# Kernel optimization log

Measured on AMD Instinct MI355X. Metric: run time of the kernel, lower is better.

Reference implementation:

```python
import jax, jax.numpy as jnp
import numpy as np

B, Hh, Ww, C = 64, 14, 14, 2048   # batch, feat map H, W, encoder_dim
E, D, A, V, L = 512, 512, 512, 30000, 32  # embed, decoder, attn dims, vocab, max text len
SC = 0.02


def setup_inputs() -> dict:
    key = jax.random.key(0)
    ks = jax.random.split(key, 16)
    def p(k, shape):
        return jax.random.normal(k, shape, jnp.float32) * SC
    lens = jax.random.randint(ks[2], (B, 1), 2, L + 1).at[0, 0].set(L)  # ensure max len present -> static T
    return {
        "encoder_out": jax.random.normal(ks[0], (B, Hh, Ww, C), jnp.float32),
        "encoded_text": jax.random.randint(ks[1], (B, L), 0, V),
        "encoded_text_len": lens,
        "W_init_h": p(ks[3], (C, D)), "b_init_h": jnp.zeros((D,), jnp.float32),
        "W_init_c": p(ks[4], (C, D)), "b_init_c": jnp.zeros((D,), jnp.float32),
        "W_en": p(ks[5], (C, A)), "b_en": jnp.zeros((A,), jnp.float32),
        "W_de": p(ks[6], (D, A)), "b_de": jnp.zeros((A,), jnp.float32),
        "W_at": p(ks[7], (A, 1)), "b_at": jnp.zeros((1,), jnp.float32),
        "W_gate": p(ks[8], (D, C)), "b_gate": jnp.zeros((C,), jnp.float32),
        "W_ih": p(ks[9], (C + E, 4 * D)), "b_ih": jnp.zeros((4 * D,), jnp.float32),
        "W_hh": p(ks[10], (D, 4 * D)), "b_hh": jnp.zeros((4 * D,), jnp.float32),
        "embed_table": p(ks[11], (V, E)),
        "W_head": p(ks[12], (D, V)), "b_head": jnp.zeros((V,), jnp.float32),
    }


def reference(encoder_out, encoded_text, encoded_text_len,
              W_init_h, b_init_h, W_init_c, b_init_c,
              W_en, b_en, W_de, b_de, W_at, b_at,
              W_gate, b_gate, W_ih, b_ih, W_hh, b_hh,
              embed_table, W_head, b_head):
    b, hh, ww, c = encoder_out.shape
    img = encoder_out.reshape(b, hh * ww, c)          # [b, p, c]
    img_mean = img.mean(axis=1)
    # NOTE: original computes h0/c0 on UNSORTED img and never reindexes them (repo quirk); reproduced faithfully.
    h0 = img_mean @ W_init_h + b_init_h               # [b, d]
    c0 = img_mean @ W_init_c + b_init_c
    tl = encoded_text_len[:, 0]
    idx = jnp.argsort(-tl, stable=True)               # descending stable sort
    img_s = img[idx]
    text_s = encoded_text[idx]
    tlen = tl[idx] - 1                                # decode steps per example
    T = encoded_text.shape[1] - 1                     # static: one row has full length L
    emb = embed_table[text_s[:, :T]]                  # [b, T, e]
    en_attn = img_s @ W_en + b_en                     # [b, p, a] time-invariant attn projection

    def step(carry, xs):
        h, cst = carry
        emb_t, mask = xs                              # [b,e], [b]
        de = h @ W_de + b_de                          # [b, a]
        score = (jax.nn.relu(en_attn + de[:, None, :]) @ W_at)[..., 0] + b_at[0]  # [b, p]
        alpha = jax.nn.softmax(score, axis=1)
        ctx = jnp.einsum('bp,bpc->bc', alpha, img_s)
        gate = jax.nn.sigmoid(h @ W_gate + b_gate)
        x = jnp.concatenate([ctx * gate, emb_t], axis=1)
        gates = x @ W_ih + b_ih + h @ W_hh + b_hh     # [b, 4d], torch LSTMCell gate order i,f,g,o
        i, f, g, o = jnp.split(gates, 4, axis=1)
        c_new = jax.nn.sigmoid(f) * cst + jax.nn.sigmoid(i) * jnp.tanh(g)
        h_new = jax.nn.sigmoid(o) * jnp.tanh(c_new)
        m = mask[:, None]
        h = jnp.where(m, h_new, h)
        cst = jnp.where(m, c_new, cst)
        pred = jnp.where(m, h_new @ W_head + b_head, 0.0)  # dropout in eval mode = identity
        attn = jnp.where(m, alpha, 0.0)
        return (h, cst), (pred, attn)

    emb_T = jnp.swapaxes(emb, 0, 1)                   # [T, b, e]
    masks = jnp.arange(T)[:, None] < tlen[None, :]    # [T, b] prefix-active (lengths sorted desc)
    (_, _), (preds, attns) = jax.lax.scan(step, (h0, c0), (emb_T, masks))
    prediction = jnp.swapaxes(preds, 0, 1)            # [b, T, V]
    attention = jnp.swapaxes(attns, 0, 1)             # [b, T, p]
    return prediction, text_s, tlen, attention, idx
```

## Files before the change

kernel.cpp:

```cpp
#include <hip/hip_runtime.h>
#include <hip/hip_bf16.h>
#include <math.h>

#define BB 64
#define PP 196
#define CC 2048
#define DD 512
#define AA 512
#define EE 512
#define VV 30000
#define VPAD 30016
#define LL 32
#define TT 31
#define XH 2560
#define HEADBLK 469

typedef short bf16x8 __attribute__((ext_vector_type(8)));
typedef float f32x4 __attribute__((ext_vector_type(4)));

__device__ inline unsigned short f2bf(float x) {
    __hip_bfloat16 h = __float2bfloat16(x);
    return __builtin_bit_cast(unsigned short, h);
}
__device__ inline float bf2f(unsigned short u) {
    unsigned int x = ((unsigned int)u) << 16;
    return __builtin_bit_cast(float, x);
}

template<int K, int LDA>
__device__ inline void mm4(const unsigned short* __restrict__ a0,
                           const unsigned short* __restrict__ b0,
                           f32x4 acc[4]) {
#pragma unroll
    for (int kc = 0; kc < K / 32; ++kc) {
        bf16x8 bfr = *reinterpret_cast<const bf16x8*>(b0 + kc * 32);
#pragma unroll
        for (int mt = 0; mt < 4; ++mt) {
            bf16x8 afr = *reinterpret_cast<const bf16x8*>(a0 + (size_t)mt * 16 * LDA + kc * 32);
            acc[mt] = __builtin_amdgcn_mfma_f32_16x16x32_bf16(afr, bfr, acc[mt], 0, 0, 0);
        }
    }
}


__global__ void k_sort(const int* __restrict__ text, const int* __restrict__ lens,
                       int* __restrict__ idx, int* __restrict__ inv, int* __restrict__ tlen,
                       int* __restrict__ ts,
                       float* __restrict__ out_text, float* __restrict__ out_tlen,
                       float* __restrict__ out_idx) {
    int j = threadIdx.x;
    __shared__ int key[BB];
    __shared__ int sidx[BB];
    key[j] = lens[j];
    __syncthreads();
    int kj = key[j];
    int pos = 0;
    for (int q = 0; q < BB; ++q) {
        int kq = key[q];
        if (kq > kj || (kq == kj && q < j)) pos++;
    }
    sidx[pos] = j;
    __syncthreads();
    int src = sidx[j];
    idx[j] = src;
    inv[src] = j;
    int tl = key[src] - 1;
    tlen[j] = tl;
    out_idx[j] = (float)src;
    out_tlen[j] = (float)tl;
    for (int l = 0; l < LL; ++l) {
        int tok = text[src * LL + l];
        ts[j * LL + l] = tok;
        out_text[j * LL + l] = (float)tok;
    }
}

__global__ __launch_bounds__(256) void k_cvtenc(const float* __restrict__ enc, const int* __restrict__ idx,
                                                unsigned short* __restrict__ enc_bf) {
    int row = blockIdx.x;
    int bs = row / PP, p = row - bs * PP;
    int c0 = threadIdx.x * 8;
    const float* src = enc + ((size_t)idx[bs] * PP + p) * CC + c0;
    f32x4 lo = *reinterpret_cast<const f32x4*>(src);
    f32x4 hi = *reinterpret_cast<const f32x4*>(src + 4);
    unsigned short* dst = enc_bf + (size_t)row * CC + c0;
    bf16x8 v;
    v[0] = (short)f2bf(lo[0]); v[1] = (short)f2bf(lo[1]);
    v[2] = (short)f2bf(lo[2]); v[3] = (short)f2bf(lo[3]);
    v[4] = (short)f2bf(hi[0]); v[5] = (short)f2bf(hi[1]);
    v[6] = (short)f2bf(hi[2]); v[7] = (short)f2bf(hi[3]);
    *reinterpret_cast<bf16x8*>(dst) = v;
}

__global__ __launch_bounds__(256) void k_meanbf(const unsigned short* __restrict__ enc_bf,
                                                const int* __restrict__ inv,
                                                unsigned short* __restrict__ mean_bf) {
    int b = blockIdx.x;
    int lane = threadIdx.x & 31, pg = threadIdx.x >> 5;
    int c0 = blockIdx.y * 256 + lane * 8;
    const unsigned short* img = enc_bf + (size_t)inv[b] * PP * CC + c0;
    float s[8] = {0.f, 0.f, 0.f, 0.f, 0.f, 0.f, 0.f, 0.f};
    for (int p = pg; p < PP; p += 8) {
        bf16x8 v = *reinterpret_cast<const bf16x8*>(img + (size_t)p * CC);
#pragma unroll
        for (int j = 0; j < 8; ++j) s[j] += bf2f((unsigned short)v[j]);
    }
    __shared__ float red[8][256];
#pragma unroll
    for (int j = 0; j < 8; ++j) red[pg][lane * 8 + j] = s[j];
    __syncthreads();
    int c = threadIdx.x;
    float tt = 0.f;
#pragma unroll
    for (int g = 0; g < 8; ++g) tt += red[g][c];
    mean_bf[(size_t)b * CC + blockIdx.y * 256 + c] = f2bf(tt * (1.0f / PP));
}

__global__ __launch_bounds__(64) void k_init_mfma(const unsigned short* __restrict__ mean_bf,
                                                  const unsigned short* __restrict__ Wt_ih,
                                                  const unsigned short* __restrict__ Wt_ic,
                                                  const float* __restrict__ bh, const float* __restrict__ bc,
                                                  unsigned short* __restrict__ xh_bf, float* __restrict__ c_f32) {
    int isC = blockIdx.x >= 32;
    int n0 = (blockIdx.x & 31) * 16;
    int lane = threadIdx.x;
    const unsigned short* Wt = isC ? Wt_ic : Wt_ih;
    const unsigned short* a0 = mean_bf + (size_t)(lane & 15) * CC + ((lane >> 4) * 8);
    const unsigned short* b0 = Wt + (size_t)(n0 + (lane & 15)) * CC + ((lane >> 4) * 8);
    f32x4 acc[4];
#pragma unroll
    for (int mt = 0; mt < 4; ++mt) acc[mt] = (f32x4){0.f, 0.f, 0.f, 0.f};
    mm4<CC, CC>(a0, b0, acc);
    int n = n0 + (lane & 15);
    float bv = (isC ? bc : bh)[n];
#pragma unroll
    for (int mt = 0; mt < 4; ++mt)
#pragma unroll
        for (int r = 0; r < 4; ++r) {
            int m = mt * 16 + (lane >> 4) * 4 + r;
            float val = acc[mt][r] + bv;
            if (isC) c_f32[(size_t)m * DD + n] = val;
            else     xh_bf[(size_t)m * XH + CC + n] = f2bf(val);
        }
}

__global__ __launch_bounds__(256) void k_transcvt(const float* __restrict__ src, int K, int N,
                                                  unsigned short* __restrict__ dst, int dstStride, int Npad) {
    __shared__ float t[32][33];
    int n0 = blockIdx.x * 32, k0 = blockIdx.y * 32;
    int tx = threadIdx.x, ty = threadIdx.y;
#pragma unroll
    for (int r = 0; r < 4; ++r) {
        int k = k0 + ty + r * 8;
        int n = n0 + tx;
        t[ty + r * 8][tx] = (n < N) ? src[(size_t)k * N + n] : 0.f;
    }
    __syncthreads();
#pragma unroll
    for (int r = 0; r < 4; ++r) {
        int n = n0 + ty + r * 8;
        int k = k0 + tx;
        if (n < Npad) dst[(size_t)n * dstStride + k] = f2bf(t[tx][ty + r * 8]);
    }
}

__global__ __launch_bounds__(256) void k_emball(const float* __restrict__ embed, const int* __restrict__ ts,
                                                unsigned short* __restrict__ emb_all) {
    int row = blockIdx.x;
    int t = row >> 6, b = row & 63;
    int tok = ts[b * LL + t];
    int e = threadIdx.x * 2;
    const float* src = embed + (size_t)tok * EE + e;
    unsigned short* dst = emb_all + (size_t)row * EE + e;
    dst[0] = f2bf(src[0]);
    dst[1] = f2bf(src[1]);
}

__global__ __launch_bounds__(256) void k_embw(const unsigned short* __restrict__ emb_all,
                                              const unsigned short* __restrict__ Wt_emb,
                                              const float* __restrict__ bih, const float* __restrict__ bhh,
                                              float* __restrict__ embW) {
    int tstep = blockIdx.x;
    int n0 = blockIdx.y * 64;
    int lane = threadIdx.x & 63, w = threadIdx.x >> 6;
    const unsigned short* a0 = emb_all + ((size_t)tstep * 64 + (lane & 15)) * EE + ((lane >> 4) * 8);
    const unsigned short* b0 = Wt_emb + (size_t)(n0 + w * 16 + (lane & 15)) * EE + ((lane >> 4) * 8);
    f32x4 acc[4];
#pragma unroll
    for (int mt = 0; mt < 4; ++mt) acc[mt] = (f32x4){0.f, 0.f, 0.f, 0.f};
    mm4<EE, EE>(a0, b0, acc);
    int n = n0 + w * 16 + (lane & 15);
    float bv = bih[n] + bhh[n];
#pragma unroll
    for (int mt = 0; mt < 4; ++mt)
#pragma unroll
        for (int r = 0; r < 4; ++r) {
            int m = mt * 16 + (lane >> 4) * 4 + r;
            embW[((size_t)tstep * 64 + m) * 2048 + n] = acc[mt][r] + bv;
        }
}

__global__ __launch_bounds__(256) void k_enattn_mfma(const unsigned short* __restrict__ enc_bf,
                                                     const unsigned short* __restrict__ Wt,
                                                     const float* __restrict__ bias,
                                                     unsigned short* __restrict__ en_bf) {
    int m0 = blockIdx.x * 64;
    int lane = threadIdx.x & 63, w = threadIdx.x >> 6;
    const unsigned short* a0 = enc_bf + (size_t)(m0 + (lane & 15)) * CC + ((lane >> 4) * 8);
    const unsigned short* bptr[8];
#pragma unroll
    for (int nt = 0; nt < 8; ++nt) {
        int rowB = nt * 64 + w * 16 + (lane & 15);
        bptr[nt] = Wt + (size_t)rowB * CC + ((lane >> 4) * 8);
    }
    f32x4 acc[4][8];
#pragma unroll
    for (int mt = 0; mt < 4; ++mt)
#pragma unroll
        for (int nt = 0; nt < 8; ++nt) acc[mt][nt] = (f32x4){0.f, 0.f, 0.f, 0.f};

    for (int kc = 0; kc < CC / 32; ++kc) {
        bf16x8 afr[4];
#pragma unroll
        for (int mt = 0; mt < 4; ++mt)
            afr[mt] = *reinterpret_cast<const bf16x8*>(a0 + (size_t)mt * 16 * CC + kc * 32);
#pragma unroll
        for (int nt = 0; nt < 8; ++nt) {
            bf16x8 bfr = *reinterpret_cast<const bf16x8*>(bptr[nt] + kc * 32);
#pragma unroll
            for (int mt = 0; mt < 4; ++mt)
                acc[mt][nt] = __builtin_amdgcn_mfma_f32_16x16x32_bf16(afr[mt], bfr, acc[mt][nt], 0, 0, 0);
        }
    }
#pragma unroll
    for (int nt = 0; nt < 8; ++nt) {
        int n = nt * 64 + w * 16 + (lane & 15);
        float bv = bias[n];
#pragma unroll
        for (int mt = 0; mt < 4; ++mt)
#pragma unroll
            for (int r = 0; r < 4; ++r) {
                int m = m0 + mt * 16 + (lane >> 4) * 4 + r;
                en_bf[(size_t)m * AA + n] = f2bf(acc[mt][nt][r] + bv);
            }
    }
}


__global__ __launch_bounds__(256) void k_de0(const unsigned short* __restrict__ xh_bf,
                                             const unsigned short* __restrict__ Wt,
                                             const float* __restrict__ bias, float* __restrict__ de) {
    int lane = threadIdx.x & 63, w = threadIdx.x >> 6;
    int n0 = (blockIdx.x * 4 + w) * 16;
    const unsigned short* a0 = xh_bf + CC + (size_t)(lane & 15) * XH + ((lane >> 4) * 8);
    const unsigned short* b0 = Wt + (size_t)(n0 + (lane & 15)) * DD + ((lane >> 4) * 8);
    f32x4 acc[4];
#pragma unroll
    for (int mt = 0; mt < 4; ++mt) acc[mt] = (f32x4){0.f, 0.f, 0.f, 0.f};
    mm4<DD, XH>(a0, b0, acc);
    int n = n0 + (lane & 15);
    float bv = bias[n];
#pragma unroll
    for (int mt = 0; mt < 4; ++mt)
#pragma unroll
        for (int r = 0; r < 4; ++r) {
            int m = mt * 16 + (lane >> 4) * 4 + r;
            de[(size_t)m * AA + n] = acc[mt][r] + bv;
        }
}

__global__ __launch_bounds__(256) void k_score(const unsigned short* __restrict__ en_bf,
                                               const float* __restrict__ de,
                                               const float* __restrict__ Wat, const float* __restrict__ bat,
                                               const int* __restrict__ tlen, int t,
                                               float* __restrict__ alpha, float* __restrict__ out_attn) {
    int b = blockIdx.x;
    int tid = threadIdx.x;
    __shared__ float deL[AA];
    __shared__ float watL[AA];
    __shared__ float red[256];
    deL[tid] = de[(size_t)b * AA + tid];
    deL[tid + 256] = de[(size_t)b * AA + 256 + tid];
    watL[tid] = Wat[tid];
    watL[tid + 256] = Wat[tid + 256];
    __syncthreads();
    float s0 = 0.f, s1 = 0.f;
    if (tid < PP) {
        const unsigned short* er = en_bf + ((size_t)b * PP + tid) * AA;
#pragma unroll 2
        for (int a16 = 0; a16 < AA / 16; ++a16) {
            bf16x8 v0 = *reinterpret_cast<const bf16x8*>(er + a16 * 16);
            bf16x8 v1 = *reinterpret_cast<const bf16x8*>(er + a16 * 16 + 8);
#pragma unroll
            for (int j = 0; j < 8; ++j) {
                float u0 = fmaxf(bf2f((unsigned short)v0[j]) + deL[a16 * 16 + j], 0.f);
                float u1 = fmaxf(bf2f((unsigned short)v1[j]) + deL[a16 * 16 + 8 + j], 0.f);
                s0 = fmaf(u0, watL[a16 * 16 + j], s0);
                s1 = fmaf(u1, watL[a16 * 16 + 8 + j], s1);
            }
        }
    }
    float s = s0 + s1 + bat[0];
    red[tid] = (tid < PP) ? s : -3.4e38f;
    __syncthreads();
    for (int st = 128; st > 0; st >>= 1) {
        if (tid < st) red[tid] = fmaxf(red[tid], red[tid + st]);
        __syncthreads();
    }
    float m = red[0];
    __syncthreads();
    float e = (tid < PP) ? expf(s - m) : 0.f;
    red[tid] = e;
    __syncthreads();
    for (int st = 128; st > 0; st >>= 1) {
        if (tid < st) red[tid] += red[tid + st];
        __syncthreads();
    }
    float inv = 1.0f / red[0];
    if (tid < PP) {
        float al = e * inv;
        alpha[(size_t)b * PP + tid] = al;
        bool act = t < tlen[b];
        out_attn[((size_t)b * TT + t) * PP + tid] = act ? al : 0.f;
    }
}

__global__ __launch_bounds__(256) void k_ctx(const unsigned short* __restrict__ enc_bf,
                                             const float* __restrict__ alpha, float* __restrict__ ctx) {
    int b = blockIdx.x;
    int lane = threadIdx.x & 31, pg = threadIdx.x >> 5;
    int c0 = blockIdx.y * 256 + lane * 8;
    __shared__ float al[PP];
    if (threadIdx.x < PP) al[threadIdx.x] = alpha[(size_t)b * PP + threadIdx.x];
    __syncthreads();
    const unsigned short* img = enc_bf + (size_t)b * PP * CC + c0;
    float s[8] = {0.f, 0.f, 0.f, 0.f, 0.f, 0.f, 0.f, 0.f};
    for (int p = pg; p < PP; p += 8) {
        float a = al[p];
        bf16x8 v = *reinterpret_cast<const bf16x8*>(img + (size_t)p * CC);
#pragma unroll
        for (int j = 0; j < 8; ++j) s[j] = fmaf(a, bf2f((unsigned short)v[j]), s[j]);
    }
    __shared__ float red[8][256];
#pragma unroll
    for (int j = 0; j < 8; ++j) red[pg][lane * 8 + j] = s[j];
    __syncthreads();
    int c = threadIdx.x;
    float tt = 0.f;
#pragma unroll
    for (int g = 0; g < 8; ++g) tt += red[g][c];
    ctx[(size_t)b * CC + blockIdx.y * 256 + c] = tt;
}

__global__ __launch_bounds__(64) void k_gatex_mfma(unsigned short* __restrict__ xh_bf,
                                                   const unsigned short* __restrict__ Wt,
                                                   const float* __restrict__ bias,
                                                   const float* __restrict__ ctx) {
    int n0 = blockIdx.x * 16;
    int lane = threadIdx.x;
    const unsigned short* a0 = xh_bf + CC + (size_t)(lane & 15) * XH + ((lane >> 4) * 8);
    const unsigned short* b0 = Wt + (size_t)(n0 + (lane & 15)) * DD + ((lane >> 4) * 8);
    f32x4 acc[4];
#pragma unroll
    for (int mt = 0; mt < 4; ++mt) acc[mt] = (f32x4){0.f, 0.f, 0.f, 0.f};
    mm4<DD, XH>(a0, b0, acc);
    int n = n0 + (lane & 15);
    float bv = bias[n];
#pragma unroll
    for (int mt = 0; mt < 4; ++mt)
#pragma unroll
        for (int r = 0; r < 4; ++r) {
            int m = mt * 16 + (lane >> 4) * 4 + r;
            float g = 1.f / (1.f + expf(-(acc[mt][r] + bv)));
            xh_bf[(size_t)m * XH + n] = f2bf(ctx[(size_t)m * CC + n] * g);
        }
}

__global__ __launch_bounds__(64) void k_gateslstm(const unsigned short* __restrict__ xh_bf,
                                                  const unsigned short* __restrict__ Wt,
                                                  const float* __restrict__ embW,
                                                  const int* __restrict__ tlen, int t,
                                                  unsigned short* __restrict__ xh_out,
                                                  float* __restrict__ c_f32,
                                                  unsigned short* __restrict__ hn_bf) {
    int d0 = blockIdx.x * 16;
    int lane = threadIdx.x;
    int col = lane & 15;
    const unsigned short* a0 = xh_bf + (size_t)col * XH + ((lane >> 4) * 8);
    const unsigned short* bptr[4];
#pragma unroll
    for (int g = 0; g < 4; ++g)
        bptr[g] = Wt + (size_t)(g * DD + d0 + col) * XH + ((lane >> 4) * 8);

    f32x4 acc[4][4];
    const float* ew = embW + (size_t)t * 64 * 2048;
#pragma unroll
    for (int g = 0; g < 4; ++g)
#pragma unroll
        for (int mt = 0; mt < 4; ++mt)
#pragma unroll
            for (int r = 0; r < 4; ++r) {
                int m = mt * 16 + (lane >> 4) * 4 + r;
                acc[g][mt][r] = ew[(size_t)m * 2048 + g * DD + d0 + col];
            }

#pragma unroll 4
    for (int kc = 0; kc < XH / 32; ++kc) {
        bf16x8 afr[4];
#pragma unroll
        for (int mt = 0; mt < 4; ++mt)
            afr[mt] = *reinterpret_cast<const bf16x8*>(a0 + (size_t)mt * 16 * XH + kc * 32);
#pragma unroll
        for (int g = 0; g < 4; ++g) {
            bf16x8 bfr = *reinterpret_cast<const bf16x8*>(bptr[g] + kc * 32);
#pragma unroll
            for (int mt = 0; mt < 4; ++mt)
                acc[g][mt] = __builtin_amdgcn_mfma_f32_16x16x32_bf16(afr[mt], bfr, acc[g][mt], 0, 0, 0);
        }
    }

    int d = d0 + col;
#pragma unroll
    for (int mt = 0; mt < 4; ++mt)
#pragma unroll
        for (int r = 0; r < 4; ++r) {
            int b = mt * 16 + (lane >> 4) * 4 + r;
            float iv = acc[0][mt][r], fv = acc[1][mt][r], gv = acc[2][mt][r], ov = acc[3][mt][r];
            float cv = c_f32[(size_t)b * DD + d];
            float si = 1.f / (1.f + expf(-iv));
            float sf = 1.f / (1.f + expf(-fv));
            float so = 1.f / (1.f + expf(-ov));
            float cn = sf * cv + si * tanhf(gv);
            float hn = so * tanhf(cn);
            hn_bf[(size_t)b * DD + d] = f2bf(hn);
            if (t < tlen[b]) {
                xh_out[(size_t)b * XH + CC + d] = f2bf(hn);
                c_f32[(size_t)b * DD + d] = cn;
            }
        }
}

__global__ __launch_bounds__(256) void k_head_de(const unsigned short* __restrict__ hn_bf,
                                                 const unsigned short* __restrict__ Wt_head,
                                                 const float* __restrict__ b_head,
                                                 const unsigned short* __restrict__ xh_bf,
                                                 const unsigned short* __restrict__ Wt_de,
                                                 const float* __restrict__ b_de,
                                                 const int* __restrict__ tlen, int t,
                                                 float* __restrict__ out_pred, float* __restrict__ de) {
    int lane = threadIdx.x & 63, w = threadIdx.x >> 6;
    if (blockIdx.x < HEADBLK) {
        int n0 = blockIdx.x * 64;
        const unsigned short* a0 = hn_bf + (size_t)(lane & 15) * DD + ((lane >> 4) * 8);
        const unsigned short* b0 = Wt_head + (size_t)(n0 + w * 16 + (lane & 15)) * DD + ((lane >> 4) * 8);
        f32x4 acc[4];
#pragma unroll
        for (int mt = 0; mt < 4; ++mt) acc[mt] = (f32x4){0.f, 0.f, 0.f, 0.f};
        mm4<DD, DD>(a0, b0, acc);
        int v = n0 + w * 16 + (lane & 15);
        if (v >= VV) return;
        float bv = b_head[v];
#pragma unroll
        for (int mt = 0; mt < 4; ++mt)
#pragma unroll
            for (int r = 0; r < 4; ++r) {
                int b = mt * 16 + (lane >> 4) * 4 + r;
                bool act = t < tlen[b];
                out_pred[(size_t)b * TT * VV + (size_t)t * VV + v] = act ? (acc[mt][r] + bv) : 0.f;
            }
    } else {
        int n0 = ((blockIdx.x - HEADBLK) * 4 + w) * 16;
        const unsigned short* a0 = xh_bf + CC + (size_t)(lane & 15) * XH + ((lane >> 4) * 8);
        const unsigned short* b0 = Wt_de + (size_t)(n0 + (lane & 15)) * DD + ((lane >> 4) * 8);
        f32x4 acc[4];
#pragma unroll
        for (int mt = 0; mt < 4; ++mt) acc[mt] = (f32x4){0.f, 0.f, 0.f, 0.f};
        mm4<DD, XH>(a0, b0, acc);
        int n = n0 + (lane & 15);
        float bv = b_de[n];
#pragma unroll
        for (int mt = 0; mt < 4; ++mt)
#pragma unroll
            for (int r = 0; r < 4; ++r) {
                int m = mt * 16 + (lane >> 4) * 4 + r;
                de[(size_t)m * AA + n] = acc[mt][r] + bv;
            }
    }
}

extern "C" void kernel_launch(void* const* d_in, const int* in_sizes, int n_in,
                              void* d_out, int out_size, void* d_ws, size_t ws_size,
                              hipStream_t stream) {
    const float* enc     = (const float*)d_in[0];
    const int*   text    = (const int*)d_in[1];
    const int*   lens    = (const int*)d_in[2];
    const float* W_init_h = (const float*)d_in[3];
    const float* b_init_h = (const float*)d_in[4];
    const float* W_init_c = (const float*)d_in[5];
    const float* b_init_c = (const float*)d_in[6];
    const float* W_en    = (const float*)d_in[7];
    const float* b_en    = (const float*)d_in[8];
    const float* W_de    = (const float*)d_in[9];
    const float* b_de    = (const float*)d_in[10];
    const float* W_at    = (const float*)d_in[11];
    const float* b_at    = (const float*)d_in[12];
    const float* W_gate  = (const float*)d_in[13];
    const float* b_gate  = (const float*)d_in[14];
    const float* W_ih    = (const float*)d_in[15];
    const float* b_ih    = (const float*)d_in[16];
    const float* W_hh    = (const float*)d_in[17];
    const float* b_hh    = (const float*)d_in[18];
    const float* embed   = (const float*)d_in[19];
    const float* W_head  = (const float*)d_in[20];
    const float* b_head  = (const float*)d_in[21];

    float* outf = (float*)d_out;
    float* out_pred = outf;
    float* out_text = outf + (size_t)BB * TT * VV;
    float* out_tlen = out_text + BB * LL;
    float* out_attn = out_tlen + BB;
    float* out_idx  = out_attn + (size_t)BB * TT * PP;

    char* wsb = (char*)d_ws;
    int* idx  = (int*)wsb;
    int* inv  = idx + 64;
    int* tlen = inv + 64;
    int* ts   = tlen + 64;
    float* fw = (float*)(wsb + 16384);
    float* c_f32 = fw;  fw += (size_t)BB * DD;
    float* de    = fw;  fw += (size_t)BB * AA;
    float* alpha = fw;  fw += (size_t)BB * PP;
    float* ctx   = fw;  fw += (size_t)BB * CC;
    float* embW  = fw;  fw += (size_t)TT * BB * 2048;
    unsigned short* us = (unsigned short*)fw;
    unsigned short* mean_bf = us;  us += (size_t)BB * CC;
    unsigned short* xh_bf   = us;  us += (size_t)BB * XH;
    unsigned short* hn_bf   = us;  us += (size_t)BB * DD;
    unsigned short* emb_all = us;  us += (size_t)TT * BB * EE;
    unsigned short* en_bf   = us;  us += (size_t)BB * PP * AA;
    unsigned short* enc_bf  = us;  us += (size_t)BB * PP * CC;
    unsigned short* Wt_en   = us;  us += (size_t)AA * CC;
    unsigned short* Wt_de   = us;  us += (size_t)AA * DD;
    unsigned short* Wt_gate = us;  us += (size_t)CC * DD;
    unsigned short* Wt_emb  = us;  us += (size_t)2048 * EE;
    unsigned short* Wt_ihh  = us;  us += (size_t)2048 * XH;
    unsigned short* Wt_ih0  = us;  us += (size_t)DD * CC;
    unsigned short* Wt_ic0  = us;  us += (size_t)DD * CC;
    unsigned short* Wt_head = us;  us += (size_t)VPAD * DD;

    k_sort<<<1, 64, 0, stream>>>(text, lens, idx, inv, tlen, ts, out_text, out_tlen, out_idx);
    k_cvtenc<<<BB * PP, 256, 0, stream>>>(enc, idx, enc_bf);
    k_meanbf<<<dim3(BB, CC / 256), 256, 0, stream>>>(enc_bf, inv, mean_bf);

    dim3 tb(32, 8);
    k_transcvt<<<dim3(AA / 32, CC / 32), tb, 0, stream>>>(W_en, CC, AA, Wt_en, CC, AA);
    k_transcvt<<<dim3(AA / 32, DD / 32), tb, 0, stream>>>(W_de, DD, AA, Wt_de, DD, AA);
    k_transcvt<<<dim3(CC / 32, DD / 32), tb, 0, stream>>>(W_gate, DD, CC, Wt_gate, DD, CC);
    k_transcvt<<<dim3(CC / 32, CC / 32), tb, 0, stream>>>(W_ih, CC, 2048, Wt_ihh, XH, 2048);
    k_transcvt<<<dim3(CC / 32, DD / 32), tb, 0, stream>>>(W_hh, DD, 2048, Wt_ihh + CC, XH, 2048);
    k_transcvt<<<dim3(CC / 32, DD / 32), tb, 0, stream>>>(W_ih + (size_t)CC * 2048, DD, 2048, Wt_emb, EE, 2048);
    k_transcvt<<<dim3(DD / 32, CC / 32), tb, 0, stream>>>(W_init_h, CC, DD, Wt_ih0, CC, DD);
    k_transcvt<<<dim3(DD / 32, CC / 32), tb, 0, stream>>>(W_init_c, CC, DD, Wt_ic0, CC, DD);
    k_transcvt<<<dim3(VPAD / 32, DD / 32), tb, 0, stream>>>(W_head, DD, VV, Wt_head, DD, VPAD);

    k_init_mfma<<<64, 64, 0, stream>>>(mean_bf, Wt_ih0, Wt_ic0, b_init_h, b_init_c, xh_bf, c_f32);
    k_emball<<<TT * BB, 256, 0, stream>>>(embed, ts, emb_all);
    k_embw<<<dim3(TT, 2048 / 64), 256, 0, stream>>>(emb_all, Wt_emb, b_ih, b_hh, embW);
    k_enattn_mfma<<<PP, 256, 0, stream>>>(enc_bf, Wt_en, b_en, en_bf);
    k_de0<<<8, 256, 0, stream>>>(xh_bf, Wt_de, b_de, de);

    for (int t = 0; t < TT; ++t) {
        k_score<<<BB, 256, 0, stream>>>(en_bf, de, W_at, b_at, tlen, t, alpha, out_attn);
        k_ctx<<<dim3(BB, 8), 256, 0, stream>>>(enc_bf, alpha, ctx);
        k_gatex_mfma<<<CC / 16, 64, 0, stream>>>(xh_bf, Wt_gate, b_gate, ctx);
        k_gateslstm<<<DD / 16, 64, 0, stream>>>(xh_bf, Wt_ihh, embW, tlen, t, xh_bf, c_f32, hn_bf);
        k_head_de<<<HEADBLK + 8, 256, 0, stream>>>(hn_bf, Wt_head, b_head, xh_bf, Wt_de, b_de,
                                                   tlen, t, out_pred, de);
    }
}
```

Measured before the change: 3.091 ms.

## Fuse attention score, softmax and context; skip inactive rows in per-step GEMMs

```diff
diff --git a/kernel.cpp b/kernel.cpp
--- a/kernel.cpp
+++ b/kernel.cpp
@@ -38,6 +38,23 @@
         for (int mt = 0; mt < 4; ++mt) {
             bf16x8 afr = *reinterpret_cast<const bf16x8*>(a0 + (size_t)mt * 16 * LDA + kc * 32);
             acc[mt] = __builtin_amdgcn_mfma_f32_16x16x32_bf16(afr, bfr, acc[mt], 0, 0, 0);
+        }
+    }
+}
+
+template<int K, int LDA>
+__device__ inline void mm4s(const unsigned short* __restrict__ a0,
+                            const unsigned short* __restrict__ b0,
+                            const bool act[4], f32x4 acc[4]) {
+#pragma unroll 4
+    for (int kc = 0; kc < K / 32; ++kc) {
+        bf16x8 bfr = *reinterpret_cast<const bf16x8*>(b0 + kc * 32);
+#pragma unroll
+        for (int mt = 0; mt < 4; ++mt) {
+            if (act[mt]) {
+                bf16x8 afr = *reinterpret_cast<const bf16x8*>(a0 + (size_t)mt * 16 * LDA + kc * 32);
+                acc[mt] = __builtin_amdgcn_mfma_f32_16x16x32_bf16(afr, bfr, acc[mt], 0, 0, 0);
+            }
         }
     }
 }
@@ -246,71 +263,103 @@
     }
 }
 
-
-__global__ __launch_bounds__(256) void k_de0(const unsigned short* __restrict__ xh_bf,
-                                             const unsigned short* __restrict__ Wt,
-                                             const float* __restrict__ bias, float* __restrict__ de) {
+__global__ __launch_bounds__(256) void k_pre0(const unsigned short* __restrict__ xh_bf,
+                                              const unsigned short* __restrict__ Wt_de,
+                                              const float* __restrict__ b_de,
+                                              const unsigned short* __restrict__ Wt_gate,
+                                              const float* __restrict__ b_gate,
+                                              float* __restrict__ de, float* __restrict__ gsig) {
     int lane = threadIdx.x & 63, w = threadIdx.x >> 6;
-    int n0 = (blockIdx.x * 4 + w) * 16;
-    const unsigned short* a0 = xh_bf + CC + (size_t)(lane & 15) * XH + ((lane >> 4) * 8);
-    const unsigned short* b0 = Wt + (size_t)(n0 + (lane & 15)) * DD + ((lane >> 4) * 8);
+    int l15 = lane & 15, hi = lane >> 4;
+    const unsigned short* a0 = xh_bf + CC + (size_t)l15 * XH + hi * 8;
     f32x4 acc[4];
 #pragma unroll
     for (int mt = 0; mt < 4; ++mt) acc[mt] = (f32x4){0.f, 0.f, 0.f, 0.f};
-    mm4<DD, XH>(a0, b0, acc);
-    int n = n0 + (lane & 15);
-    float bv = bias[n];
-#pragma unroll
-    for (int mt = 0; mt < 4; ++mt)
-#pragma unroll
-        for (int r = 0; r < 4; ++r) {
-            int m = mt * 16 + (lane >> 4) * 4 + r;
-            de[(size_t)m * AA + n] = acc[mt][r] + bv;
-        }
-}
-
-__global__ __launch_bounds__(256) void k_score(const unsigned short* __restrict__ en_bf,
+    if (blockIdx.x < 8) {
+        int n0 = (blockIdx.x * 4 + w) * 16;
+        const unsigned short* b0 = Wt_de + (size_t)(n0 + l15) * DD + hi * 8;
+        mm4<DD, XH>(a0, b0, acc);
+        int n = n0 + l15;
+        float bv = b_de[n];
+#pragma unroll
+        for (int mt = 0; mt < 4; ++mt)
+#pragma unroll
+            for (int r = 0; r < 4; ++r) {
+                int m = mt * 16 + hi * 4 + r;
+                de[(size_t)m * AA + n] = acc[mt][r] + bv;
+            }
+    } else {
+        int n0 = (blockIdx.x - 8) * 64 + w * 16;
+        const unsigned short* b0 = Wt_gate + (size_t)(n0 + l15) * DD + hi * 8;
+        mm4<DD, XH>(a0, b0, acc);
+        int n = n0 + l15;
+        float bv = b_gate[n];
+#pragma unroll
+        for (int mt = 0; mt < 4; ++mt)
+#pragma unroll
+            for (int r = 0; r < 4; ++r) {
+                int m = mt * 16 + hi * 4 + r;
+                gsig[(size_t)m * CC + n] = 1.f / (1.f + expf(-(acc[mt][r] + bv)));
+            }
+    }
+}
+
+
+__global__ __launch_bounds__(1024) void k_attn(const unsigned short* __restrict__ en_bf,
                                                const float* __restrict__ de,
                                                const float* __restrict__ Wat, const float* __restrict__ bat,
                                                const int* __restrict__ tlen, int t,
-                                               float* __restrict__ alpha, float* __restrict__ out_attn) {
-    int b = blockIdx.x;
-    int tid = threadIdx.x;
+                                               const unsigned short* __restrict__ enc_bf,
+                                               const float* __restrict__ gsig,
+                                               unsigned short* __restrict__ xh_bf,
+                                               float* __restrict__ out_attn) {
+    int b = blockIdx.x, tid = threadIdx.x;
+    if (t >= tlen[b]) {
+        if (tid < PP) out_attn[((size_t)b * TT + t) * PP + tid] = 0.f;
+        return;
+    }
     __shared__ float deL[AA];
     __shared__ float watL[AA];
+    __shared__ float sred[256][4];
+    __shared__ float sL[256];
     __shared__ float red[256];
-    deL[tid] = de[(size_t)b * AA + tid];
-    deL[tid + 256] = de[(size_t)b * AA + 256 + tid];
-    watL[tid] = Wat[tid];
-    watL[tid + 256] = Wat[tid + 256];
-    __syncthreads();
-    float s0 = 0.f, s1 = 0.f;
-    if (tid < PP) {
-        const unsigned short* er = en_bf + ((size_t)b * PP + tid) * AA;
-#pragma unroll 2
-        for (int a16 = 0; a16 < AA / 16; ++a16) {
-            bf16x8 v0 = *reinterpret_cast<const bf16x8*>(er + a16 * 16);
-            bf16x8 v1 = *reinterpret_cast<const bf16x8*>(er + a16 * 16 + 8);
+    __shared__ float red4[4][2048];
+    if (tid < 512) { deL[tid] = de[(size_t)b * AA + tid]; watL[tid] = Wat[tid]; }
+    __syncthreads();
+    int row = tid >> 2, ch = tid & 3;
+    float s = 0.f;
+    if (row < PP) {
+        const unsigned short* er = en_bf + ((size_t)b * PP + row) * AA + ch * 128;
+#pragma unroll
+        for (int a8 = 0; a8 < 16; ++a8) {
+            bf16x8 v = *reinterpret_cast<const bf16x8*>(er + a8 * 8);
 #pragma unroll
             for (int j = 0; j < 8; ++j) {
-                float u0 = fmaxf(bf2f((unsigned short)v0[j]) + deL[a16 * 16 + j], 0.f);
-                float u1 = fmaxf(bf2f((unsigned short)v1[j]) + deL[a16 * 16 + 8 + j], 0.f);
-                s0 = fmaf(u0, watL[a16 * 16 + j], s0);
-                s1 = fmaf(u1, watL[a16 * 16 + 8 + j], s1);
-            }
-        }
-    }
-    float s = s0 + s1 + bat[0];
-    red[tid] = (tid < PP) ? s : -3.4e38f;
+                int ix = ch * 128 + a8 * 8 + j;
+                float u = fmaxf(bf2f((unsigned short)v[j]) + deL[ix], 0.f);
+                s = fmaf(u, watL[ix], s);
+            }
+        }
+    }
+    sred[row][ch] = s;
+    __syncthreads();
+    float sc = 0.f;
+    if (tid < 256) {
+        sc = sred[tid][0] + sred[tid][1] + sred[tid][2] + sred[tid][3] + bat[0];
+        red[tid] = (tid < PP) ? sc : -3.4e38f;
+    }
     __syncthreads();
     for (int st = 128; st > 0; st >>= 1) {
         if (tid < st) red[tid] = fmaxf(red[tid], red[tid + st]);
         __syncthreads();
     }
-    float m = red[0];
-    __syncthreads();
-    float e = (tid < PP) ? expf(s - m) : 0.f;
-    red[tid] = e;
+    float mx = red[0];
+    __syncthreads();
+    if (tid < 256) {
+        float e = (tid < PP) ? expf(sc - mx) : 0.f;
+        sL[tid] = e;
+        red[tid] = e;
+    }
     __syncthreads();
     for (int st = 128; st > 0; st >>= 1) {
         if (tid < st) red[tid] += red[tid + st];
@@ -318,172 +367,160 @@
     }
     float inv = 1.0f / red[0];
     if (tid < PP) {
-        float al = e * inv;
-        alpha[(size_t)b * PP + tid] = al;
-        bool act = t < tlen[b];
-        out_attn[((size_t)b * TT + t) * PP + tid] = act ? al : 0.f;
-    }
-}
-
-__global__ __launch_bounds__(256) void k_ctx(const unsigned short* __restrict__ enc_bf,
-                                             const float* __restrict__ alpha, float* __restrict__ ctx) {
-    int b = blockIdx.x;
-    int lane = threadIdx.x & 31, pg = threadIdx.x >> 5;
-    int c0 = blockIdx.y * 256 + lane * 8;
-    __shared__ float al[PP];
-    if (threadIdx.x < PP) al[threadIdx.x] = alpha[(size_t)b * PP + threadIdx.x];
-    __syncthreads();
+        float al = sL[tid] * inv;
+        sL[tid] = al;
+        out_attn[((size_t)b * TT + t) * PP + tid] = al;
+    }
+    __syncthreads();
+    int lane8 = tid & 255, pg = tid >> 8;
+    int c0 = lane8 * 8;
     const unsigned short* img = enc_bf + (size_t)b * PP * CC + c0;
-    float s[8] = {0.f, 0.f, 0.f, 0.f, 0.f, 0.f, 0.f, 0.f};
-    for (int p = pg; p < PP; p += 8) {
-        float a = al[p];
+    float s8[8] = {0.f, 0.f, 0.f, 0.f, 0.f, 0.f, 0.f, 0.f};
+    for (int p = pg; p < PP; p += 4) {
+        float a = sL[p];
         bf16x8 v = *reinterpret_cast<const bf16x8*>(img + (size_t)p * CC);
 #pragma unroll
-        for (int j = 0; j < 8; ++j) s[j] = fmaf(a, bf2f((unsigned short)v[j]), s[j]);
-    }
-    __shared__ float red[8][256];
-#pragma unroll
-    for (int j = 0; j < 8; ++j) red[pg][lane * 8 + j] = s[j];
-    __syncthreads();
-    int c = threadIdx.x;
-    float tt = 0.f;
-#pragma unroll
-    for (int g = 0; g < 8; ++g) tt += red[g][c];
-    ctx[(size_t)b * CC + blockIdx.y * 256 + c] = tt;
-}
-
-__global__ __launch_bounds__(64) void k_gatex_mfma(unsigned short* __restrict__ xh_bf,
+        for (int j = 0; j < 8; ++j) s8[j] = fmaf(a, bf2f((unsigned short)v[j]), s8[j]);
+    }
+#pragma unroll
+    for (int j = 0; j < 8; ++j) red4[pg][c0 + j] = s8[j];
+    __syncthreads();
+    for (int c = tid; c < CC; c += 1024) {
+        float v = red4[0][c] + red4[1][c] + red4[2][c] + red4[3][c];
+        xh_bf[(size_t)b * XH + c] = f2bf(v * gsig[(size_t)b * CC + c]);
+    }
+}
+
+__global__ __launch_bounds__(256) void k_gateslstm(const unsigned short* __restrict__ xh_bf,
                                                    const unsigned short* __restrict__ Wt,
-                                                   const float* __restrict__ bias,
-                                                   const float* __restrict__ ctx) {
-    int n0 = blockIdx.x * 16;
-    int lane = threadIdx.x;
-    const unsigned short* a0 = xh_bf + CC + (size_t)(lane & 15) * XH + ((lane >> 4) * 8);
-    const unsigned short* b0 = Wt + (size_t)(n0 + (lane & 15)) * DD + ((lane >> 4) * 8);
+                                                   const float* __restrict__ embW,
+                                                   const int* __restrict__ tlen, int t,
+                                                   unsigned short* __restrict__ xh_out,
+                                                   float* __restrict__ c_f32,
+                                                   unsigned short* __restrict__ hn_bf) {
+    int d0 = blockIdx.x * 16;
+    int tid = threadIdx.x, wid = tid >> 6, lane = tid & 63;
+    int l15 = lane & 15, hi = lane >> 4;
+    bool act[4];
+#pragma unroll
+    for (int mt = 0; mt < 4; ++mt) act[mt] = t < tlen[mt * 16];
+
+    const unsigned short* a0 = xh_bf + (size_t)l15 * XH + hi * 8;
+    const unsigned short* b0 = Wt + (size_t)(wid * DD + d0 + l15) * XH + hi * 8;
+
     f32x4 acc[4];
+    const float* ew = embW + (size_t)t * 64 * 2048;
+#pragma unroll
+    for (int mt = 0; mt < 4; ++mt)
+#pragma unroll
+        for (int r = 0; r < 4; ++r) {
+            int m = mt * 16 + hi * 4 + r;
+            acc[mt][r] = ew[(size_t)m * 2048 + wid * DD + d0 + l15];
+        }
+    mm4s<XH, XH>(a0, b0, act, acc);
+
+    __shared__ float lg[4][64][16];
+#pragma unroll
+    for (int mt = 0; mt < 4; ++mt)
+#pragma unroll
+        for (int r = 0; r < 4; ++r) lg[wid][lane][mt * 4 + r] = acc[mt][r];
+    __syncthreads();
+    if (wid == 0) {
+        int d = d0 + l15;
+#pragma unroll
+        for (int mt = 0; mt < 4; ++mt) {
+            if (!act[mt]) continue;
+#pragma unroll
+            for (int r = 0; r < 4; ++r) {
+                int b = mt * 16 + hi * 4 + r;
+                float iv = lg[0][lane][mt * 4 + r];
+                float fv = lg[1][lane][mt * 4 + r];
+                float gv = lg[2][lane][mt * 4 + r];
+                float ov = lg[3][lane][mt * 4 + r];
+                float cv = c_f32[(size_t)b * DD + d];
+                float si = 1.f / (1.f + expf(-iv));
+                float sf = 1.f / (1.f + expf(-fv));
+                float so = 1.f / (1.f + expf(-ov));
+                float cn = sf * cv + si * tanhf(gv);
+                float hn = so * tanhf(cn);
+                hn_bf[(size_t)b * DD + d] = f2bf(hn);
+                if (t < tlen[b]) {
+                    xh_out[(size_t)b * XH + CC + d] = f2bf(hn);
+                    c_f32[(size_t)b * DD + d] = cn;
+                }
+            }
+        }
+    }
+}
+
+__global__ __launch_bounds__(256) void k_head_de_gate(const unsigned short* __restrict__ hn_bf,
+                                                      const unsigned short* __restrict__ Wt_head,
+                                                      const float* __restrict__ b_head,
+                                                      const unsigned short* __restrict__ xh_bf,
+                                                      const unsigned short* __restrict__ Wt_de,
+                                                      const float* __restrict__ b_de,
+                                                      const unsigned short* __restrict__ Wt_gate,
+                                                      const float* __restrict__ b_gate,
+                                                      const int* __restrict__ tlen, int t,
+                                                      float* __restrict__ out_pred,
+                                                      float* __restrict__ de, float* __restrict__ gsig) {
+    int lane = threadIdx.x & 63, w = threadIdx.x >> 6;
+    int l15 = lane & 15, hi = lane >> 4;
+    f32x4 acc[4];
 #pragma unroll
     for (int mt = 0; mt < 4; ++mt) acc[mt] = (f32x4){0.f, 0.f, 0.f, 0.f};
-    mm4<DD, XH>(a0, b0, acc);
-    int n = n0 + (lane & 15);
-    float bv = bias[n];
-#pragma unroll
-    for (int mt = 0; mt < 4; ++mt)
-#pragma unroll
-        for (int r = 0; r < 4; ++r) {
-            int m = mt * 16 + (lane >> 4) * 4 + r;
-            float g = 1.f / (1.f + expf(-(acc[mt][r] + bv)));
-            xh_bf[(size_t)m * XH + n] = f2bf(ctx[(size_t)m * CC + n] * g);
-        }
-}
-
-__global__ __launch_bounds__(64) void k_gateslstm(const unsigned short* __restrict__ xh_bf,
-                                                  const unsigned short* __restrict__ Wt,
-                                                  const float* __restrict__ embW,
-                                                  const int* __restrict__ tlen, int t,
-                                                  unsigned short* __restrict__ xh_out,
-                                                  float* __restrict__ c_f32,
-                                                  unsigned short* __restrict__ hn_bf) {
-    int d0 = blockIdx.x * 16;
-    int lane = threadIdx.x;
-    int col = lane & 15;
-    const unsigned short* a0 = xh_bf + (size_t)col * XH + ((lane >> 4) * 8);
-    const unsigned short* bptr[4];
-#pragma unroll
-    for (int g = 0; g < 4; ++g)
-        bptr[g] = Wt + (size_t)(g * DD + d0 + col) * XH + ((lane >> 4) * 8);
-
-    f32x4 acc[4][4];
-    const float* ew = embW + (size_t)t * 64 * 2048;
-#pragma unroll
-    for (int g = 0; g < 4; ++g)
-#pragma unroll
-        for (int mt = 0; mt < 4; ++mt)
-#pragma unroll
-            for (int r = 0; r < 4; ++r) {
-                int m = mt * 16 + (lane >> 4) * 4 + r;
-                acc[g][mt][r] = ew[(size_t)m * 2048 + g * DD + d0 + col];
-            }
-
-#pragma unroll 4
-    for (int kc = 0; kc < XH / 32; ++kc) {
-        bf16x8 afr[4];
-#pragma unroll
-        for (int mt = 0; mt < 4; ++mt)
-            afr[mt] = *reinterpret_cast<const bf16x8*>(a0 + (size_t)mt * 16 * XH + kc * 32);
-#pragma unroll
-        for (int g = 0; g < 4; ++g) {
-            bf16x8 bfr = *reinterpret_cast<const bf16x8*>(bptr[g] + kc * 32);
-#pragma unroll
-            for (int mt = 0; mt < 4; ++mt)
-                acc[g][mt] = __builtin_amdgcn_mfma_f32_16x16x32_bf16(afr[mt], bfr, acc[g][mt], 0, 0, 0);
-        }
-    }
-
-    int d = d0 + col;
-#pragma unroll
-    for (int mt = 0; mt < 4; ++mt)
-#pragma unroll
-        for (int r = 0; r < 4; ++r) {
-            int b = mt * 16 + (lane >> 4) * 4 + r;
-            float iv = acc[0][mt][r], fv = acc[1][mt][r], gv = acc[2][mt][r], ov = acc[3][mt][r];
-            float cv = c_f32[(size_t)b * DD + d];
-            float si = 1.f / (1.f + expf(-iv));
-            float sf = 1.f / (1.f + expf(-fv));
-            float so = 1.f / (1.f + expf(-ov));
-            float cn = sf * cv + si * tanhf(gv);
-            float hn = so * tanhf(cn);
-            hn_bf[(size_t)b * DD + d] = f2bf(hn);
-            if (t < tlen[b]) {
-                xh_out[(size_t)b * XH + CC + d] = f2bf(hn);
-                c_f32[(size_t)b * DD + d] = cn;
-            }
-        }
-}
-
-__global__ __launch_bounds__(256) void k_head_de(const unsigned short* __restrict__ hn_bf,
-                                                 const unsigned short* __restrict__ Wt_head,
-                                                 const float* __restrict__ b_head,
-                                                 const unsigned short* __restrict__ xh_bf,
-                                                 const unsigned short* __restrict__ Wt_de,
-                                                 const float* __restrict__ b_de,
-                                                 const int* __restrict__ tlen, int t,
-                                                 float* __restrict__ out_pred, float* __restrict__ de) {
-    int lane = threadIdx.x & 63, w = threadIdx.x >> 6;
     if (blockIdx.x < HEADBLK) {
+        bool act[4];
+#pragma unroll
+        for (int mt = 0; mt < 4; ++mt) act[mt] = t < tlen[mt * 16];
         int n0 = blockIdx.x * 64;
-        const unsigned short* a0 = hn_bf + (size_t)(lane & 15) * DD + ((lane >> 4) * 8);
-        const unsigned short* b0 = Wt_head + (size_t)(n0 + w * 16 + (lane & 15)) * DD + ((lane >> 4) * 8);
-        f32x4 acc[4];
-#pragma unroll
-        for (int mt = 0; mt < 4; ++mt) acc[mt] = (f32x4){0.f, 0.f, 0.f, 0.f};
-        mm4<DD, DD>(a0, b0, acc);
-        int v = n0 + w * 16 + (lane & 15);
+        const unsigned short* a0 = hn_bf + (size_t)l15 * DD + hi * 8;
+        const unsigned short* b0 = Wt_head + (size_t)(n0 + w * 16 + l15) * DD + hi * 8;
+        mm4s<DD, DD>(a0, b0, act, acc);
+        int v = n0 + w * 16 + l15;
         if (v >= VV) return;
         float bv = b_head[v];
 #pragma unroll
         for (int mt = 0; mt < 4; ++mt)
 #pragma unroll
             for (int r = 0; r < 4; ++r) {
-                int b = mt * 16 + (lane >> 4) * 4 + r;
-                bool act = t < tlen[b];
-                out_pred[(size_t)b * TT * VV + (size_t)t * VV + v] = act ? (acc[mt][r] + bv) : 0.f;
+                int b = mt * 16 + hi * 4 + r;
+                bool a = t < tlen[b];
+                out_pred[(size_t)b * TT * VV + (size_t)t * VV + v] = a ? (acc[mt][r] + bv) : 0.f;
+            }
+    } else if (blockIdx.x < HEADBLK + 8) {
+        bool act[4];
+#pragma unroll
+        for (int mt = 0; mt < 4; ++mt) act[mt] = (t + 1) < tlen[mt * 16];
+        int n0 = ((blockIdx.x - HEADBLK) * 4 + w) * 16;
+        const unsigned short* a0 = xh_bf + CC + (size_t)l15 * XH + hi * 8;
+        const unsigned short* b0 = Wt_de + (size_t)(n0 + l15) * DD + hi * 8;
+        mm4s<DD, XH>(a0, b0, act, acc);
+        int n = n0 + l15;
+        float bv = b_de[n];
+#pragma unroll
+        for (int mt = 0; mt < 4; ++mt)
+#pragma unroll
+            for (int r = 0; r < 4; ++r) {
+                int m = mt * 16 + hi * 4 + r;
+                de[(size_t)m * AA + n] = acc[mt][r] + bv;
             }
     } else {
-        int n0 = ((blockIdx.x - HEADBLK) * 4 + w) * 16;
-        const unsigned short* a0 = xh_bf + CC + (size_t)(lane & 15) * XH + ((lane >> 4) * 8);
-        const unsigned short* b0 = Wt_de + (size_t)(n0 + (lane & 15)) * DD + ((lane >> 4) * 8);
-        f32x4 acc[4];
-#pragma unroll
-        for (int mt = 0; mt < 4; ++mt) acc[mt] = (f32x4){0.f, 0.f, 0.f, 0.f};
-        mm4<DD, XH>(a0, b0, acc);
-        int n = n0 + (lane & 15);
-        float bv = b_de[n];
+        bool act[4];
+#pragma unroll
+        for (int mt = 0; mt < 4; ++mt) act[mt] = (t + 1) < tlen[mt * 16];
+        int n0 = (blockIdx.x - HEADBLK - 8) * 64 + w * 16;
+        const unsigned short* a0 = xh_bf + CC + (size_t)l15 * XH + hi * 8;
+        const unsigned short* b0 = Wt_gate + (size_t)(n0 + l15) * DD + hi * 8;
+        mm4s<DD, XH>(a0, b0, act, acc);
+        int n = n0 + l15;
+        float bv = b_gate[n];
 #pragma unroll
         for (int mt = 0; mt < 4; ++mt)
 #pragma unroll
             for (int r = 0; r < 4; ++r) {
-                int m = mt * 16 + (lane >> 4) * 4 + r;
-                de[(size_t)m * AA + n] = acc[mt][r] + bv;
+                int m = mt * 16 + hi * 4 + r;
+                gsig[(size_t)m * CC + n] = 1.f / (1.f + expf(-(acc[mt][r] + bv)));
             }
     }
 }
@@ -529,8 +566,7 @@
     float* fw = (float*)(wsb + 16384);
     float* c_f32 = fw;  fw += (size_t)BB * DD;
     float* de    = fw;  fw += (size_t)BB * AA;
-    float* alpha = fw;  fw += (size_t)BB * PP;
-    float* ctx   = fw;  fw += (size_t)BB * CC;
+    float* gsig  = fw;  fw += (size_t)BB * CC;
     float* embW  = fw;  fw += (size_t)TT * BB * 2048;
     unsigned short* us = (unsigned short*)fw;
     unsigned short* mean_bf = us;  us += (size_t)BB * CC;
@@ -567,14 +603,12 @@
     k_emball<<<TT * BB, 256, 0, stream>>>(embed, ts, emb_all);
     k_embw<<<dim3(TT, 2048 / 64), 256, 0, stream>>>(emb_all, Wt_emb, b_ih, b_hh, embW);
     k_enattn_mfma<<<PP, 256, 0, stream>>>(enc_bf, Wt_en, b_en, en_bf);
-    k_de0<<<8, 256, 0, stream>>>(xh_bf, Wt_de, b_de, de);
+    k_pre0<<<40, 256, 0, stream>>>(xh_bf, Wt_de, b_de, Wt_gate, b_gate, de, gsig);
 
     for (int t = 0; t < TT; ++t) {
-        k_score<<<BB, 256, 0, stream>>>(en_bf, de, W_at, b_at, tlen, t, alpha, out_attn);
-        k_ctx<<<dim3(BB, 8), 256, 0, stream>>>(enc_bf, alpha, ctx);
-        k_gatex_mfma<<<CC / 16, 64, 0, stream>>>(xh_bf, Wt_gate, b_gate, ctx);
-        k_gateslstm<<<DD / 16, 64, 0, stream>>>(xh_bf, Wt_ihh, embW, tlen, t, xh_bf, c_f32, hn_bf);
-        k_head_de<<<HEADBLK + 8, 256, 0, stream>>>(hn_bf, Wt_head, b_head, xh_bf, Wt_de, b_de,
-                                                   tlen, t, out_pred, de);
-    }
-}
+        k_attn<<<BB, 1024, 0, stream>>>(en_bf, de, W_at, b_at, tlen, t, enc_bf, gsig, xh_bf, out_attn);
+        k_gateslstm<<<DD / 16, 256, 0, stream>>>(xh_bf, Wt_ihh, embW, tlen, t, xh_bf, c_f32, hn_bf);
+        k_head_de_gate<<<HEADBLK + 40, 256, 0, stream>>>(hn_bf, Wt_head, b_head, xh_bf, Wt_de, b_de,
+                                                         Wt_gate, b_gate, tlen, t, out_pred, de, gsig);
+    }
+}
```

New measurement: 3.916 ms. 1.27x slower.
